# Kernel tuning notes

Hardware: AMD Instinct MI355X
Metric: run time of the kernel (lower is better)

The kernel has to match this reference:

```python
import jax, jax.numpy as jnp
import numpy as np

N, HEADS, OUT = 8192, 4, 64  # hidden = HEADS*OUT = 256
DIN = 256
NEG = -9e15
ALPHA = 0.2


def setup_inputs() -> dict:
    key = jax.random.key(0)
    ks = jax.random.split(key, 6)
    X = jax.random.normal(ks[0], (N, DIN), dtype=jnp.float32)
    A = jax.random.randint(ks[1], (N, N), 0, 2, dtype=jnp.int32)  # dense 0/1 adjacency
    hid = HEADS * OUT
    W = jax.random.normal(ks[2], (hid, DIN), dtype=jnp.float32) * 0.05  # nn.Linear weight [out,in]
    b = jax.random.normal(ks[3], (hid,), dtype=jnp.float32) * 0.05
    a_s = jax.random.normal(ks[4], (hid, 1), dtype=jnp.float32) * 0.05
    a_r = jax.random.normal(ks[5], (hid, 1), dtype=jnp.float32) * 0.05
    return {"X": X, "A": A, "W": W, "b": b, "a_s": a_s, "a_r": a_r}


def reference(X, A, W, b, a_s, a_r):
    Af = A.astype(jnp.float32)
    H_in = X @ W.T + b                      # [N, hid]
    s = H_in @ a_s                          # [N, 1]
    r = H_in @ a_r                          # [N, 1]
    M = Af * s + Af * r.T                   # M_s + M_r, [N, N]
    scores = jax.nn.leaky_relu(M, negative_slope=ALPHA)
    masked = jnp.where(Af > 0, scores, jnp.float32(NEG))
    C = jax.nn.softmax(masked, axis=1)      # row softmax; dropout = identity (eval)
    H_out = C @ H_in                        # [N, hid]; act = Identity, LayerNorm output discarded
    H_final = H_out.reshape(N, HEADS, OUT).sum(axis=1)  # concat='sum'
    return H_final
```

## Files before the change

### kernel.cpp

```cpp
#include <hip/hip_runtime.h>

typedef __attribute__((ext_vector_type(8))) short short8;
typedef __attribute__((ext_vector_type(4))) short short4v;
typedef __attribute__((ext_vector_type(4))) float f32x4;
typedef __attribute__((ext_vector_type(4))) int i32x4;

#define NN 8192
#define ALPHA 0.2f

__device__ __forceinline__ float bf16_to_f32(unsigned short h) {
    union { unsigned int u; float f; } c;
    c.u = ((unsigned int)h) << 16;
    return c.f;
}
__device__ __forceinline__ unsigned short f32_to_bf16(float f) {
    union { float f; unsigned int u; } c;
    c.f = f;
    unsigned int r = (c.u + 0x7FFFu + ((c.u >> 16) & 1u)) >> 16;
    return (unsigned short)r;
}
__device__ __forceinline__ unsigned short f32_to_bf16_fast(float f) {
    union { float f; unsigned int u; } c;
    c.f = f;
    return (unsigned short)((c.u + 0x8000u) >> 16);
}

__device__ __forceinline__ int probe_isbf16(const void* Xv, int tid) {
    __shared__ int wsum[4];
    const unsigned short* x16 = (const unsigned short*)Xv;
    int cnt = 0;
#pragma unroll
    for (int j = 0; j < 4; j++) {
        float v = bf16_to_f32(x16[tid * 4 + j]);
        float a = fabsf(v);
        if (a > 1e-6f && a < 64.0f) cnt++;
    }
#pragma unroll
    for (int m = 1; m <= 32; m <<= 1) cnt += __shfl_xor(cnt, m, 64);
    if ((tid & 63) == 0) wsum[tid >> 6] = cnt;
    __syncthreads();
    return (wsum[0] + wsum[1] + wsum[2] + wsum[3]) > 800;
}

__global__ __launch_bounds__(256) void gat_prep(
    const void* __restrict__ Xv, const void* __restrict__ Wv,
    const void* __restrict__ bv, const void* __restrict__ asv,
    const void* __restrict__ arv,
    short* __restrict__ Xb, short* __restrict__ Wb,
    float* __restrict__ bF, float* __restrict__ asF, float* __restrict__ arF,
    int* __restrict__ flagOut) {
    const int tid = threadIdx.x;
    const int isBf = probe_isbf16(Xv, tid);
    if (blockIdx.x == 0 && tid == 0) *flagOut = isBf;

    const int GX = NN * 256 / 8;
    const int GW = 256 * 256 / 8;
    const int idx = blockIdx.x * 256 + tid;
    const int stride = 256 * 256;
    for (int i = idx; i < GX + GW; i += stride) {
        const void* src = (i < GX) ? Xv : Wv;
        short* dst = (i < GX) ? Xb : Wb;
        int g = (i < GX) ? i : i - GX;
        short8 o;
        if (isBf) {
            o = ((const short8*)src)[g];
        } else {
            f32x4 a = ((const f32x4*)src)[2 * g];
            f32x4 b = ((const f32x4*)src)[2 * g + 1];
#pragma unroll
            for (int j = 0; j < 4; j++) {
                o[j] = (short)f32_to_bf16(a[j]);
                o[4 + j] = (short)f32_to_bf16(b[j]);
            }
        }
        ((short8*)dst)[g] = o;
    }
    if (idx < 768) {
        int which = idx >> 8;
        int k = idx & 255;
        const void* src = (which == 0) ? bv : (which == 1) ? asv : arv;
        float v = isBf ? bf16_to_f32(((const unsigned short*)src)[k])
                       : ((const float*)src)[k];
        float* dst = (which == 0) ? bF : (which == 1) ? asF : arF;
        dst[k] = v;
    }
}

__global__ __launch_bounds__(128) void gat_gemm1(
    const short* __restrict__ Xb, const short* __restrict__ Wb,
    const float* __restrict__ bF, const float* __restrict__ asF,
    const float* __restrict__ arF,
    short* __restrict__ Gfrag, float* __restrict__ sOut, float* __restrict__ rOut) {
    __shared__ short Gl[64][32];
    const int tid = threadIdx.x;
    const int wave = tid >> 6, lane = tid & 63;
    const int l15 = lane & 15, lhi = lane >> 4;
    const int rowBase = blockIdx.x * 32 + wave * 16;

    f32x4 acc[16];
#pragma unroll
    for (int n = 0; n < 16; n++) acc[n] = (f32x4){0.f, 0.f, 0.f, 0.f};

    const short8* Xrow = (const short8*)(Xb + (size_t)(rowBase + l15) * 256);
#pragma unroll
    for (int ks = 0; ks < 8; ks++) {
        short8 a = Xrow[ks * 4 + lhi];
#pragma unroll
        for (int n = 0; n < 16; n++) {
            const short8* Wrow = (const short8*)(Wb + (size_t)(n * 16 + l15) * 256);
            short8 bf = Wrow[ks * 4 + lhi];
            acc[n] = __builtin_amdgcn_mfma_f32_16x16x32_bf16(a, bf, acc[n], 0, 0, 0);
        }
    }

    float sPart[4] = {0.f, 0.f, 0.f, 0.f};
    float rPart[4] = {0.f, 0.f, 0.f, 0.f};
    float g[4][4];
#pragma unroll
    for (int na = 0; na < 4; na++)
#pragma unroll
        for (int q = 0; q < 4; q++) g[na][q] = 0.f;

#pragma unroll
    for (int n = 0; n < 16; n++) {
        int col = n * 16 + l15;
        float bias = bF[col], asc = asF[col], arc = arF[col];
#pragma unroll
        for (int q = 0; q < 4; q++) {
            float h = acc[n][q] + bias;
            sPart[q] += h * asc;
            rPart[q] += h * arc;
            g[n & 3][q] += h;
        }
    }

#pragma unroll
    for (int na = 0; na < 4; na++)
#pragma unroll
        for (int q = 0; q < 4; q++)
            Gl[na * 16 + l15][wave * 16 + lhi * 4 + q] = (short)f32_to_bf16(g[na][q]);

#pragma unroll
    for (int m = 1; m <= 8; m <<= 1) {
#pragma unroll
        for (int q = 0; q < 4; q++) {
            sPart[q] += __shfl_xor(sPart[q], m, 64);
            rPart[q] += __shfl_xor(rPart[q], m, 64);
        }
    }
    if (l15 == 0) {
#pragma unroll
        for (int q = 0; q < 4; q++) {
            int row = rowBase + lhi * 4 + q;
            sOut[row] = sPart[q];
            rOut[row] = rPart[q];
        }
    }

    __syncthreads();
    const int t_ = blockIdx.x >> 1, h_ = blockIdx.x & 1;
#pragma unroll
    for (int e = tid; e < 256; e += 128) {
        int n_ = e >> 6, le = e & 63;
        short8 v = *(const short8*)(&Gl[n_ * 16 + (le & 15)][(le >> 4) * 8]);
        *(short8*)(Gfrag + ((size_t)t_ * 8 + h_ * 4 + n_) * 512 + le * 8) = v;
    }
}


#define GAT_LOADA(AR, T_)                                                    \
    {                                                                        \
        const int* pA0_ = ab0 + (size_t)(T_) * 64;                           \
        const int* pA1_ = ab1 + (size_t)(T_) * 64;                           \
        AR[0] = *(const i32x4*)(pA0_);                                       \
        AR[1] = *(const i32x4*)(pA0_ + NN);                                  \
        AR[2] = *(const i32x4*)(pA0_ + 2 * NN);                              \
        AR[3] = *(const i32x4*)(pA0_ + 3 * NN);                              \
        AR[4] = *(const i32x4*)(pA1_);                                       \
        AR[5] = *(const i32x4*)(pA1_ + NN);                                  \
        AR[6] = *(const i32x4*)(pA1_ + 2 * NN);                              \
        AR[7] = *(const i32x4*)(pA1_ + 3 * NN);                              \
    }

#define GAT_LOADG(GR, T_)                                                    \
    {                                                                        \
        const short* bp_ = Gfrag + (size_t)(T_) * 4096 + lane * 8;           \
        GR[0] = *(const short8*)(bp_);                                       \
        GR[1] = *(const short8*)(bp_ + 512);                                 \
        GR[2] = *(const short8*)(bp_ + 1024);                                \
        GR[3] = *(const short8*)(bp_ + 1536);                                \
        GR[4] = *(const short8*)(bp_ + 2048);                                \
        GR[5] = *(const short8*)(bp_ + 2560);                                \
        GR[6] = *(const short8*)(bp_ + 3072);                                \
        GR[7] = *(const short8*)(bp_ + 3584);                                \
    }

#define GAT_BAL(Q0, Q1, Q2, Q3, V0, V1, V2, V3)                              \
    {                                                                        \
        unsigned long long W00 = __ballot((V0)[0] != 0);                     \
        unsigned long long W01 = __ballot((V0)[1] != 0);                     \
        unsigned long long W02 = __ballot((V0)[2] != 0);                     \
        unsigned long long W03 = __ballot((V0)[3] != 0);                     \
        unsigned long long W10 = __ballot((V1)[0] != 0);                     \
        unsigned long long W11 = __ballot((V1)[1] != 0);                     \
        unsigned long long W12 = __ballot((V1)[2] != 0);                     \
        unsigned long long W13 = __ballot((V1)[3] != 0);                     \
        unsigned long long W20 = __ballot((V2)[0] != 0);                     \
        unsigned long long W21 = __ballot((V2)[1] != 0);                     \
        unsigned long long W22 = __ballot((V2)[2] != 0);                     \
        unsigned long long W23 = __ballot((V2)[3] != 0);                     \
        unsigned long long W30 = __ballot((V3)[0] != 0);                     \
        unsigned long long W31 = __ballot((V3)[1] != 0);                     \
        unsigned long long W32 = __ballot((V3)[2] != 0);                     \
        unsigned long long W33 = __ballot((V3)[3] != 0);                     \
        unsigned long long w0_ = r3 == 0 ? W00 : r3 == 1 ? W10               \
                               : r3 == 2 ? W20 : W30;                        \
        unsigned long long w1_ = r3 == 0 ? W01 : r3 == 1 ? W11               \
                               : r3 == 2 ? W21 : W31;                        \
        unsigned long long w2_ = r3 == 0 ? W02 : r3 == 1 ? W12               \
                               : r3 == 2 ? W22 : W32;                        \
        unsigned long long w3_ = r3 == 0 ? W03 : r3 == 1 ? W13               \
                               : r3 == 2 ? W23 : W33;                        \
        Q0 = (unsigned int)(w0_ >> shBase);                                  \
        Q1 = (unsigned int)(w1_ >> shBase);                                  \
        Q2 = (unsigned int)(w2_ >> shBase);                                  \
        Q3 = (unsigned int)(w3_ >> shBase);                                  \
    }

#define GAT_ELEM(PA_, JP_, XV_, TW_, SH_)                                    \
    {                                                                        \
        float x_ = (XV_);                                                    \
        x_ = fmaxf(x_, ALPHA * x_);                                          \
        float e_ = __expf(x_);                                               \
        PA_[JP_] = ((TW_ >> (SH_)) & 1u) ? (short)f32_to_bf16_fast(e_)       \
                                         : (short)0;                         \
    }

#define GAT_PA(PAH0, PAH1, SM_, Q0, Q1, Q2, Q3)                              \
    {                                                                        \
        GAT_ELEM(PAH0, 0, (SM_) + ra0[0], Q0, 0)                             \
        GAT_ELEM(PAH0, 1, (SM_) + ra0[1], Q1, 0)                             \
        GAT_ELEM(PAH0, 2, (SM_) + ra0[2], Q2, 0)                             \
        GAT_ELEM(PAH0, 3, (SM_) + ra0[3], Q3, 0)                             \
        GAT_ELEM(PAH0, 4, (SM_) + ra1[0], Q0, 1)                             \
        GAT_ELEM(PAH0, 5, (SM_) + ra1[1], Q1, 1)                             \
        GAT_ELEM(PAH0, 6, (SM_) + ra1[2], Q2, 1)                             \
        GAT_ELEM(PAH0, 7, (SM_) + ra1[3], Q3, 1)                             \
        GAT_ELEM(PAH1, 0, (SM_) + rb0[0], Q0, 8)                             \
        GAT_ELEM(PAH1, 1, (SM_) + rb0[1], Q1, 8)                             \
        GAT_ELEM(PAH1, 2, (SM_) + rb0[2], Q2, 8)                             \
        GAT_ELEM(PAH1, 3, (SM_) + rb0[3], Q3, 8)                             \
        GAT_ELEM(PAH1, 4, (SM_) + rb1[0], Q0, 9)                             \
        GAT_ELEM(PAH1, 5, (SM_) + rb1[1], Q1, 9)                             \
        GAT_ELEM(PAH1, 6, (SM_) + rb1[2], Q2, 9)                             \
        GAT_ELEM(PAH1, 7, (SM_) + rb1[3], Q3, 9)                             \
    }

#define GAT_BODY(TT_, AR, GR)                                                \
    {                                                                        \
        const int k0_ = (tstart + (TT_)) * 64;                               \
        f32x4 ra0 = *(const f32x4*)(rvb + k0_);                              \
        f32x4 ra1 = *(const f32x4*)(rvb + k0_ + 4);                          \
        f32x4 rb0 = *(const f32x4*)(rvb + k0_ + 32);                         \
        f32x4 rb1 = *(const f32x4*)(rvb + k0_ + 36);                         \
        unsigned int q00, q01, q02, q03, q10, q11, q12, q13;                 \
        GAT_BAL(q00, q01, q02, q03, AR[0], AR[1], AR[2], AR[3]);             \
        GAT_BAL(q10, q11, q12, q13, AR[4], AR[5], AR[6], AR[7]);             \
        short8 pa0[2], pa1[2];                                               \
        GAT_PA(pa0[0], pa0[1], s0m, q00, q01, q02, q03);                     \
        GAT_PA(pa1[0], pa1[1], s1m, q10, q11, q12, q13);                     \
        acc[0][0] = __builtin_amdgcn_mfma_f32_16x16x32_bf16(pa0[0], GR[0],   \
                                                            acc[0][0], 0, 0, 0); \
        acc[0][1] = __builtin_amdgcn_mfma_f32_16x16x32_bf16(pa0[0], GR[1],   \
                                                            acc[0][1], 0, 0, 0); \
        acc[0][2] = __builtin_amdgcn_mfma_f32_16x16x32_bf16(pa0[0], GR[2],   \
                                                            acc[0][2], 0, 0, 0); \
        acc[0][3] = __builtin_amdgcn_mfma_f32_16x16x32_bf16(pa0[0], GR[3],   \
                                                            acc[0][3], 0, 0, 0); \
        acc[0][4] = __builtin_amdgcn_mfma_f32_16x16x32_bf16(pa0[0], onesB,   \
                                                            acc[0][4], 0, 0, 0); \
        acc[1][0] = __builtin_amdgcn_mfma_f32_16x16x32_bf16(pa1[0], GR[0],   \
                                                            acc[1][0], 0, 0, 0); \
        acc[1][1] = __builtin_amdgcn_mfma_f32_16x16x32_bf16(pa1[0], GR[1],   \
                                                            acc[1][1], 0, 0, 0); \
        acc[1][2] = __builtin_amdgcn_mfma_f32_16x16x32_bf16(pa1[0], GR[2],   \
                                                            acc[1][2], 0, 0, 0); \
        acc[1][3] = __builtin_amdgcn_mfma_f32_16x16x32_bf16(pa1[0], GR[3],   \
                                                            acc[1][3], 0, 0, 0); \
        acc[1][4] = __builtin_amdgcn_mfma_f32_16x16x32_bf16(pa1[0], onesB,   \
                                                            acc[1][4], 0, 0, 0); \
        acc[0][0] = __builtin_amdgcn_mfma_f32_16x16x32_bf16(pa0[1], GR[4],   \
                                                            acc[0][0], 0, 0, 0); \
        acc[0][1] = __builtin_amdgcn_mfma_f32_16x16x32_bf16(pa0[1], GR[5],   \
                                                            acc[0][1], 0, 0, 0); \
        acc[0][2] = __builtin_amdgcn_mfma_f32_16x16x32_bf16(pa0[1], GR[6],   \
                                                            acc[0][2], 0, 0, 0); \
        acc[0][3] = __builtin_amdgcn_mfma_f32_16x16x32_bf16(pa0[1], GR[7],   \
                                                            acc[0][3], 0, 0, 0); \
        acc[0][4] = __builtin_amdgcn_mfma_f32_16x16x32_bf16(pa0[1], onesB,   \
                                                            acc[0][4], 0, 0, 0); \
        acc[1][0] = __builtin_amdgcn_mfma_f32_16x16x32_bf16(pa1[1], GR[4],   \
                                                            acc[1][0], 0, 0, 0); \
        acc[1][1] = __builtin_amdgcn_mfma_f32_16x16x32_bf16(pa1[1], GR[5],   \
                                                            acc[1][1], 0, 0, 0); \
        acc[1][2] = __builtin_amdgcn_mfma_f32_16x16x32_bf16(pa1[1], GR[6],   \
                                                            acc[1][2], 0, 0, 0); \
        acc[1][3] = __builtin_amdgcn_mfma_f32_16x16x32_bf16(pa1[1], GR[7],   \
                                                            acc[1][3], 0, 0, 0); \
        acc[1][4] = __builtin_amdgcn_mfma_f32_16x16x32_bf16(pa1[1], onesB,   \
                                                            acc[1][4], 0, 0, 0); \
    }

__global__ __launch_bounds__(256, 2) void gat_pv9(
    const int* __restrict__ A, const short* __restrict__ Gfrag,
    const float* __restrict__ sV, const float* __restrict__ rV,
    float* __restrict__ accP, float* __restrict__ denP) {
    __shared__ float Ls[4][32][68];
    __shared__ float Ld[4][32];

    const int tid = threadIdx.x;
    const int wave = tid >> 6, lane = tid & 63;
    const int l15 = lane & 15, lhi = lane >> 4;
    const int rb = blockIdx.x >> 1;
    const int ks2 = blockIdx.x & 1;
    const int i0 = rb * 32;
    const int tstart = ks2 * 64;

    const int r3 = l15 & 3;
    const int shBase = ((l15 >> 2) << 4) + (lhi << 1);

    const float s0m = sV[i0 + l15];
    const float s1m = sV[i0 + 16 + l15];
    const int* ab0 = A + (size_t)(i0 + lhi * 4) * NN + l15 * 4 + (size_t)tstart * 64;
    const int* ab1 = ab0 + (size_t)16 * NN;
    const float* rvb = rV + lhi * 8;

    short8 onesB;
#pragma unroll
    for (int j = 0; j < 8; j++) onesB[j] = (l15 == 0) ? (short)0x3F80 : (short)0;

    f32x4 acc[2][5];
#pragma unroll
    for (int rg = 0; rg < 2; rg++)
#pragma unroll
        for (int n = 0; n < 5; n++) acc[rg][n] = (f32x4){0.f, 0.f, 0.f, 0.f};

    i32x4 aA[8], aB[8];
    short8 gA[8], gB[8];
    int tt = wave;
    GAT_LOADA(aA, tt);
    GAT_LOADG(gA, tstart + tt);
    while (tt < 64) {
        {
            const int tn = (tt + 4 < 64) ? tt + 4 : tt;
            GAT_LOADA(aB, tn);
            GAT_LOADG(gB, tstart + tn);
        }
        GAT_BODY(tt, aA, gA);
        tt += 4;
        if (tt >= 64) break;
        {
            const int tn = (tt + 4 < 64) ? tt + 4 : tt;
            GAT_LOADA(aA, tn);
            GAT_LOADG(gA, tstart + tn);
        }
        GAT_BODY(tt, aB, gB);
        tt += 4;
    }

#pragma unroll
    for (int rg = 0; rg < 2; rg++)
#pragma unroll
        for (int n = 0; n < 4; n++)
#pragma unroll
            for (int q = 0; q < 4; q++)
                Ls[wave][rg * 16 + lhi * 4 + q][n * 16 + l15] = acc[rg][n][q];
    if (l15 == 0) {
#pragma unroll
        for (int rg = 0; rg < 2; rg++)
#pragma unroll
            for (int q = 0; q < 4; q++)
                Ld[wave][rg * 16 + lhi * 4 + q] = acc[rg][4][q];
    }
    __syncthreads();

    const int row = tid >> 3, c0 = (tid & 7) * 8;
    float v[8];
#pragma unroll
    for (int j = 0; j < 8; j++)
        v[j] = Ls[0][row][c0 + j] + Ls[1][row][c0 + j] +
               Ls[2][row][c0 + j] + Ls[3][row][c0 + j];
    float* aout = accP + (size_t)ks2 * NN * 64 + (size_t)(i0 + row) * 64 + c0;
    *(f32x4*)aout = (f32x4){v[0], v[1], v[2], v[3]};
    *((f32x4*)aout + 1) = (f32x4){v[4], v[5], v[6], v[7]};
    if (tid < 32)
        denP[(size_t)ks2 * NN + i0 + tid] =
            Ld[0][tid] + Ld[1][tid] + Ld[2][tid] + Ld[3][tid];
}

__global__ void gat_final(const float* __restrict__ accP, const float* __restrict__ denP,
                          const int* __restrict__ flag, void* __restrict__ outP) {
    int idx = blockIdx.x * blockDim.x + threadIdx.x;
    if (idx >= NN * 16) return;
    int row = idx >> 4;
    float den = 0.f;
    f32x4 v = (f32x4){0.f, 0.f, 0.f, 0.f};
#pragma unroll
    for (int sk = 0; sk < 2; sk++) {
        den += denP[(size_t)sk * NN + row];
        f32x4 a = *((const f32x4*)(accP + (size_t)sk * NN * 64) + idx);
        v.x += a.x; v.y += a.y; v.z += a.z; v.w += a.w;
    }
    float inv = 1.0f / den;
    v.x *= inv; v.y *= inv; v.z *= inv; v.w *= inv;
    if (*flag) {
        short4v pk;
#pragma unroll
        for (int j = 0; j < 4; j++) pk[j] = (short)f32_to_bf16(v[j]);
        *((short4v*)outP + idx) = pk;
    } else {
        *((f32x4*)outP + idx) = v;
    }
}

extern "C" void kernel_launch(void* const* d_in, const int* in_sizes, int n_in,
                              void* d_out, int out_size, void* d_ws, size_t ws_size,
                              hipStream_t stream) {
    const void* X  = d_in[0];
    const int*  A  = (const int*)d_in[1];
    const void* W  = d_in[2];
    const void* bb = d_in[3];
    const void* as_ = d_in[4];
    const void* ar_ = d_in[5];

    char* ws = (char*)d_ws;
    const size_t OFF_FLAG = 0;
    const size_t OFF_XB   = 256;
    const size_t OFF_WB   = OFF_XB + (size_t)NN * 256 * 2;
    const size_t OFF_BF   = OFF_WB + (size_t)256 * 256 * 2;
    const size_t OFF_ASF  = OFF_BF + 1024;
    const size_t OFF_ARF  = OFF_ASF + 1024;
    const size_t OFF_S    = OFF_ARF + 1024;
    const size_t OFF_R    = OFF_S + (size_t)NN * 4;
    const size_t OFF_GF   = OFF_R + (size_t)NN * 4;
    const size_t OFF_ACC  = OFF_GF + (size_t)64 * NN * 2;
    const size_t OFF_DEN  = OFF_ACC + (size_t)2 * NN * 64 * 4;

    int*   flag = (int*)(ws + OFF_FLAG);
    short* Xb   = (short*)(ws + OFF_XB);
    short* Wb   = (short*)(ws + OFF_WB);
    float* bF   = (float*)(ws + OFF_BF);
    float* asF  = (float*)(ws + OFF_ASF);
    float* arF  = (float*)(ws + OFF_ARF);
    float* sP   = (float*)(ws + OFF_S);
    float* rP   = (float*)(ws + OFF_R);
    short* Gf   = (short*)(ws + OFF_GF);
    float* accP = (float*)(ws + OFF_ACC);
    float* denP = (float*)(ws + OFF_DEN);

    gat_prep<<<256, 256, 0, stream>>>(X, W, bb, as_, ar_, Xb, Wb, bF, asF, arF, flag);
    gat_gemm1<<<NN / 32, 128, 0, stream>>>(Xb, Wb, bF, asF, arF, Gf, sP, rP);
    gat_pv9<<<256 * 2, 256, 0, stream>>>(A, Gf, sP, rP, accP, denP);
    gat_final<<<NN * 16 / 256, 256, 0, stream>>>(accP, denP, flag, d_out);
}
```

Measured before the change: 89.17 us.

## Split PV kernel into three k-slices and single-buffer adjacency loads to raise occupancy

The attention-times-values kernel now splits the 128 column tiles across three blocks per row group instead of two, giving 768 blocks, and launch bounds ask for three blocks per CU. The adjacency prefetch drops the double-buffered register arrays and instead issues the next tile's loads right after the ballot consumes the current ones, which cuts register pressure so the higher occupancy fits. The final reduction now sums three partials, which adds a little extra partial-buffer traffic and leaves the A prefetch distance shorter.

New measurement: 80.73 us. 9.5% less time.

```diff
diff --git a/kernel.cpp b/kernel.cpp
--- a/kernel.cpp
+++ b/kernel.cpp
@@ -168,18 +168,13 @@
 }
 
 
-#define GAT_LOADA(AR, T_)                                                    \
-    {                                                                        \
-        const int* pA0_ = ab0 + (size_t)(T_) * 64;                           \
-        const int* pA1_ = ab1 + (size_t)(T_) * 64;                           \
-        AR[0] = *(const i32x4*)(pA0_);                                       \
-        AR[1] = *(const i32x4*)(pA0_ + NN);                                  \
-        AR[2] = *(const i32x4*)(pA0_ + 2 * NN);                              \
-        AR[3] = *(const i32x4*)(pA0_ + 3 * NN);                              \
-        AR[4] = *(const i32x4*)(pA1_);                                       \
-        AR[5] = *(const i32x4*)(pA1_ + NN);                                  \
-        AR[6] = *(const i32x4*)(pA1_ + 2 * NN);                              \
-        AR[7] = *(const i32x4*)(pA1_ + 3 * NN);                              \
+#define GAT_LOADA(S0, S1, S2, S3, AB_, T_)                                   \
+    {                                                                        \
+        const int* p_ = (AB_) + (size_t)(T_) * 64;                           \
+        S0 = *(const i32x4*)(p_);                                            \
+        S1 = *(const i32x4*)(p_ + NN);                                       \
+        S2 = *(const i32x4*)(p_ + 2 * NN);                                   \
+        S3 = *(const i32x4*)(p_ + 3 * NN);                                   \
     }
 
 #define GAT_LOADG(GR, T_)                                                    \
@@ -256,16 +251,22 @@
         GAT_ELEM(PAH1, 7, (SM_) + rb1[3], Q3, 9)                             \
     }
 
-#define GAT_BODY(TT_, AR, GR)                                                \
-    {                                                                        \
-        const int k0_ = (tstart + (TT_)) * 64;                               \
+#define GAT_BODY(TT_, GR)                                                    \
+    {                                                                        \
+        const int ktg_ = tstart + (TT_);                                     \
+        const int k0_ = ktg_ * 64;                                           \
         f32x4 ra0 = *(const f32x4*)(rvb + k0_);                              \
         f32x4 ra1 = *(const f32x4*)(rvb + k0_ + 4);                          \
         f32x4 rb0 = *(const f32x4*)(rvb + k0_ + 32);                         \
         f32x4 rb1 = *(const f32x4*)(rvb + k0_ + 36);                         \
         unsigned int q00, q01, q02, q03, q10, q11, q12, q13;                 \
-        GAT_BAL(q00, q01, q02, q03, AR[0], AR[1], AR[2], AR[3]);             \
-        GAT_BAL(q10, q11, q12, q13, AR[4], AR[5], AR[6], AR[7]);             \
+        GAT_BAL(q00, q01, q02, q03, s00, s01, s02, s03);                     \
+        GAT_BAL(q10, q11, q12, q13, s10, s11, s12, s13);                     \
+        {                                                                    \
+            const int tn_ = ((TT_) + 4 < tcnt) ? ktg_ + 4 : ktg_;            \
+            GAT_LOADA(s00, s01, s02, s03, ab0, tn_);                         \
+            GAT_LOADA(s10, s11, s12, s13, ab1, tn_);                         \
+        }                                                                    \
         short8 pa0[2], pa1[2];                                               \
         GAT_PA(pa0[0], pa0[1], s0m, q00, q01, q02, q03);                     \
         GAT_PA(pa1[0], pa1[1], s1m, q10, q11, q12, q13);                     \
@@ -311,7 +312,7 @@
                                                             acc[1][4], 0, 0, 0); \
     }
 
-__global__ __launch_bounds__(256, 2) void gat_pv9(
+__global__ __launch_bounds__(256, 3) void gat_pv11(
     const int* __restrict__ A, const short* __restrict__ Gfrag,
     const float* __restrict__ sV, const float* __restrict__ rV,
     float* __restrict__ accP, float* __restrict__ denP) {
@@ -321,17 +322,18 @@
     const int tid = threadIdx.x;
     const int wave = tid >> 6, lane = tid & 63;
     const int l15 = lane & 15, lhi = lane >> 4;
-    const int rb = blockIdx.x >> 1;
-    const int ks2 = blockIdx.x & 1;
+    const int rb = blockIdx.x / 3;
+    const int ks3 = blockIdx.x - rb * 3;
     const int i0 = rb * 32;
-    const int tstart = ks2 * 64;
+    const int tstart = ks3 * 43;
+    const int tcnt = (ks3 < 2) ? 43 : 42;
 
     const int r3 = l15 & 3;
     const int shBase = ((l15 >> 2) << 4) + (lhi << 1);
 
     const float s0m = sV[i0 + l15];
     const float s1m = sV[i0 + 16 + l15];
-    const int* ab0 = A + (size_t)(i0 + lhi * 4) * NN + l15 * 4 + (size_t)tstart * 64;
+    const int* ab0 = A + (size_t)(i0 + lhi * 4) * NN + l15 * 4;
     const int* ab1 = ab0 + (size_t)16 * NN;
     const float* rvb = rV + lhi * 8;
 
@@ -345,26 +347,25 @@
 #pragma unroll
         for (int n = 0; n < 5; n++) acc[rg][n] = (f32x4){0.f, 0.f, 0.f, 0.f};
 
-    i32x4 aA[8], aB[8];
+    i32x4 s00, s01, s02, s03, s10, s11, s12, s13;
     short8 gA[8], gB[8];
     int tt = wave;
-    GAT_LOADA(aA, tt);
+    GAT_LOADA(s00, s01, s02, s03, ab0, tstart + tt);
+    GAT_LOADA(s10, s11, s12, s13, ab1, tstart + tt);
     GAT_LOADG(gA, tstart + tt);
-    while (tt < 64) {
+    while (tt < tcnt) {
         {
-            const int tn = (tt + 4 < 64) ? tt + 4 : tt;
-            GAT_LOADA(aB, tn);
+            const int tn = (tt + 4 < tcnt) ? tt + 4 : tt;
             GAT_LOADG(gB, tstart + tn);
         }
-        GAT_BODY(tt, aA, gA);
+        GAT_BODY(tt, gA);
         tt += 4;
-        if (tt >= 64) break;
+        if (tt >= tcnt) break;
         {
-            const int tn = (tt + 4 < 64) ? tt + 4 : tt;
-            GAT_LOADA(aA, tn);
+            const int tn = (tt + 4 < tcnt) ? tt + 4 : tt;
             GAT_LOADG(gA, tstart + tn);
         }
-        GAT_BODY(tt, aB, gB);
+        GAT_BODY(tt, gB);
         tt += 4;
     }
 
@@ -390,11 +391,11 @@
     for (int j = 0; j < 8; j++)
         v[j] = Ls[0][row][c0 + j] + Ls[1][row][c0 + j] +
                Ls[2][row][c0 + j] + Ls[3][row][c0 + j];
-    float* aout = accP + (size_t)ks2 * NN * 64 + (size_t)(i0 + row) * 64 + c0;
+    float* aout = accP + (size_t)ks3 * NN * 64 + (size_t)(i0 + row) * 64 + c0;
     *(f32x4*)aout = (f32x4){v[0], v[1], v[2], v[3]};
     *((f32x4*)aout + 1) = (f32x4){v[4], v[5], v[6], v[7]};
     if (tid < 32)
-        denP[(size_t)ks2 * NN + i0 + tid] =
+        denP[(size_t)ks3 * NN + i0 + tid] =
             Ld[0][tid] + Ld[1][tid] + Ld[2][tid] + Ld[3][tid];
 }
 
@@ -406,7 +407,7 @@
     float den = 0.f;
     f32x4 v = (f32x4){0.f, 0.f, 0.f, 0.f};
 #pragma unroll
-    for (int sk = 0; sk < 2; sk++) {
+    for (int sk = 0; sk < 3; sk++) {
         den += denP[(size_t)sk * NN + row];
         f32x4 a = *((const f32x4*)(accP + (size_t)sk * NN * 64) + idx);
         v.x += a.x; v.y += a.y; v.z += a.z; v.w += a.w;
@@ -444,7 +445,7 @@
     const size_t OFF_R    = OFF_S + (size_t)NN * 4;
     const size_t OFF_GF   = OFF_R + (size_t)NN * 4;
     const size_t OFF_ACC  = OFF_GF + (size_t)64 * NN * 2;
-    const size_t OFF_DEN  = OFF_ACC + (size_t)2 * NN * 64 * 4;
+    const size_t OFF_DEN  = OFF_ACC + (size_t)3 * NN * 64 * 4;
 
     int*   flag = (int*)(ws + OFF_FLAG);
     short* Xb   = (short*)(ws + OFF_XB);
@@ -460,6 +461,6 @@
 
     gat_prep<<<256, 256, 0, stream>>>(X, W, bb, as_, ar_, Xb, Wb, bF, asF, arF, flag);
     gat_gemm1<<<NN / 32, 128, 0, stream>>>(Xb, Wb, bF, asF, arF, Gf, sP, rP);
-    gat_pv9<<<256 * 2, 256, 0, stream>>>(A, Gf, sP, rP, accP, denP);
+    gat_pv11<<<256 * 3, 256, 0, stream>>>(A, Gf, sP, rP, accP, denP);
     gat_final<<<NN * 16 / 256, 256, 0, stream>>>(accP, denP, flag, d_out);
 }
```
